# Kernel optimization log

Hardware: AMD Instinct MI355X
Metric: run time of the kernel (lower is better)

Reference implementation:

```python
import jax, jax.numpy as jnp
import numpy as np

S_LOCAL = 3
N_HEADS = 8
EPS = 1e-6


def setup_inputs() -> dict:
    key = jax.random.key(0)
    ks = jax.random.split(key, 9)
    B, D, T, H, W = 2, 512, 96, 16, 16
    std = 0.02
    return {
        "x": jax.random.normal(ks[0], (B, D, T, H, W), dtype=jnp.float32),
        "ln_gamma": jnp.ones((D,), dtype=jnp.float32),
        "ln_beta": jnp.zeros((D,), dtype=jnp.float32),
        "Wq": jax.random.normal(ks[1], (D, D), dtype=jnp.float32) * std,
        "Wk": jax.random.normal(ks[2], (D, D), dtype=jnp.float32) * std,
        "Wv": jax.random.normal(ks[3], (D, D), dtype=jnp.float32) * std,
        "Wkl": jax.random.normal(ks[4], (D, D), dtype=jnp.float32) * std,
        "Wvl": jax.random.normal(ks[5], (D, D), dtype=jnp.float32) * std,
        "Wo": jax.random.normal(ks[6], (D, D), dtype=jnp.float32) * std,
        "q_bias": jax.random.normal(ks[7], (1, N_HEADS, 1, D // N_HEADS), dtype=jnp.float32) * std,
    }


def _unfold_windows(x, s):
    # x: [..., T] -> [..., T, s] sliding windows with zero padding s//2 each side
    p = s // 2
    xp = jnp.pad(x, [(0, 0)] * (x.ndim - 1) + [(p, p)])
    T = x.shape[-1]
    idx = jnp.arange(T)[:, None] + jnp.arange(s)[None, :]  # [T, s]
    return xp[..., idx]


def reference(x, ln_gamma, ln_beta, Wq, Wk, Wv, Wkl, Wvl, Wo, q_bias):
    B, D, T, H, W = x.shape
    nh, dh, s = N_HEADS, D // N_HEADS, S_LOCAL
    factor = dh ** (-0.5)
    N = B * H * W

    # [B,D,T,H,W] -> [N, T, D]
    xt = jnp.transpose(x, (0, 3, 4, 2, 1)).reshape(N, T, D)

    # LayerNorm over D
    mu = xt.mean(-1, keepdims=True)
    var = xt.var(-1, keepdims=True)
    xn = (xt - mu) / jnp.sqrt(var + EPS) * ln_gamma + ln_beta

    # projections -> [N, nh, T, dh]
    def heads(y):
        return jnp.transpose(y.reshape(N, T, nh, dh), (0, 2, 1, 3))

    q = heads(xn @ Wq.T) + q_bias
    k = heads(xn @ Wk.T)
    v = heads(xn @ Wv.T)

    # global attention scores [N, nh, T, T]
    attn_global = jnp.einsum('bhnd,bhgd->bhng', q, k) * factor

    # local k/v: [N, T, D] -> [N, D, T] -> windows [N, D, T, s]
    kl = jnp.transpose(xn @ Wkl.T, (0, 2, 1))
    vl = jnp.transpose(xn @ Wvl.T, (0, 2, 1))
    k_w = jnp.transpose(_unfold_windows(kl, s).reshape(N, nh, dh, T, s), (0, 1, 3, 2, 4))  # [N,nh,T,dh,s]
    v_w = jnp.transpose(_unfold_windows(vl, s).reshape(N, nh, dh, T, s), (0, 1, 3, 2, 4))

    # local mask: True where window element came from zero padding -> [T, s]
    mask_local = _unfold_windows(jnp.ones((T,), dtype=jnp.float32), s) == 0

    attn_local = jnp.einsum('bhnd,bhndl->bhnl', q, k_w)
    attn_local = jnp.where(mask_local, -jnp.inf, attn_local) * factor

    # joint softmax over [T global + s local]
    attn_map = jax.nn.softmax(jnp.concatenate([attn_global, attn_local], axis=-1), axis=-1)
    ag, al = attn_map[..., :T], attn_map[..., T:]

    x_global = jnp.einsum('bhng,bhgd->bhnd', ag, v)
    x_local = jnp.einsum('bhnl,bhndl->bhnd', al, v_w)

    out = (jnp.transpose(x_global + x_local, (0, 2, 1, 3)).reshape(N, T, D)) @ Wo.T
    return jnp.transpose(out.reshape(B, H, W, T, D), (0, 4, 3, 1, 2))
```

## Files before the change

kernel.cpp:

```cpp
#include <hip/hip_runtime.h>
#include <hip/hip_fp16.h>
#include <cstdint>
#include <cstddef>

typedef _Float16 f16;
typedef _Float16 half8 __attribute__((ext_vector_type(8)));
typedef _Float16 half4v __attribute__((ext_vector_type(4)));
typedef float floatx4 __attribute__((ext_vector_type(4)));

#define MTOT 49152
#define QSCALE 0.180336880111120426f

__device__ __forceinline__ void gload_lds16(const f16* g, f16* l) {
  __builtin_amdgcn_global_load_lds((const __attribute__((address_space(1))) void*)g,
                                   (__attribute__((address_space(3))) void*)l, 16, 0, 0);
}

__device__ __forceinline__ half8 load_h8u(const f16* p) {
  half8 v;
  __builtin_memcpy(&v, p, 16);
  return v;
}

__global__ __launch_bounds__(256) void wconv_kernel(
    const float* __restrict__ Wq, const float* __restrict__ Wk,
    const float* __restrict__ Wv, const float* __restrict__ Wkl,
    const float* __restrict__ Wvl, const float* __restrict__ Wo,
    f16* __restrict__ WQKV, f16* __restrict__ WO) {
  int idx = blockIdx.x * 256 + threadIdx.x;
  if (idx < 2560 * 512) {
    int row = idx >> 9;
    int col = idx & 511;
    int seg = row >> 9;
    int r = row & 511;
    const float* src;
    switch (seg) {
      case 0: src = Wq; break;
      case 1: src = Wk; break;
      case 2: src = Wkl; break;
      case 3: src = Wvl; break;
      default: src = Wv; break;
    }
    WQKV[idx] = (f16)src[r * 512 + col];
  }
  if (idx < 512 * 512) WO[idx] = (f16)Wo[idx];
}

__global__ __launch_bounds__(256) void ln_kernel(
    const float* __restrict__ x, const float* __restrict__ gamma,
    const float* __restrict__ beta, f16* __restrict__ XN) {
  const int hwg = blockIdx.x & 3;
  const int t   = (blockIdx.x >> 2) % 96;
  const int b   = blockIdx.x / (4 * 96);
  const int lhw = threadIdx.x & 63;
  const int dg  = threadIdx.x >> 6;
  const float* xp = x + (size_t)b * 512 * 24576 + (size_t)t * 256 +
                    (hwg * 64 + lhw) + (size_t)dg * 128 * 24576;

  float v[128];
  float s = 0.f, s2 = 0.f;
#pragma unroll
  for (int j = 0; j < 128; ++j) {
    float u = xp[(size_t)j * 24576];
    v[j] = u;
    s += u;
    s2 += u * u;
  }
  __shared__ float S1[4][64], S2[4][64];
  __shared__ __align__(16) f16 XT[64][512];
  S1[dg][lhw] = s;
  S2[dg][lhw] = s2;
  __syncthreads();
  s  = S1[0][lhw] + S1[1][lhw] + S1[2][lhw] + S1[3][lhw];
  s2 = S2[0][lhw] + S2[1][lhw] + S2[2][lhw] + S2[3][lhw];
  const float mean = s * (1.f / 512.f);
  float var = s2 * (1.f / 512.f) - mean * mean;
  var = fmaxf(var, 0.f);
  const float rstd = rsqrtf(var + 1e-6f);

#pragma unroll
  for (int ic = 0; ic < 16; ++ic) {
    const int c = dg * 16 + ic;
    const int slot = c ^ (lhw & 7);
    half8 buf;
#pragma unroll
    for (int j = 0; j < 8; ++j) {
      const int d = c * 8 + j;
      buf[j] = (f16)((v[ic * 8 + j] - mean) * rstd * gamma[d] + beta[d]);
    }
    *(half8*)(&XT[lhw][slot * 8]) = buf;
  }
  __syncthreads();

  const int rr = threadIdx.x >> 2;
  const int seg = threadIdx.x & 3;
  const int n = b * 256 + hwg * 64 + rr;
  f16* outp = XN + ((size_t)n * 96 + t) * 512;
#pragma unroll
  for (int i = 0; i < 16; ++i) {
    const int c = i * 4 + seg;
    const int slot = c ^ (rr & 7);
    half8 w = *(const half8*)(&XT[rr][slot * 8]);
    *(half8*)(outp + c * 8) = w;
  }
}

__global__ __launch_bounds__(512, 2) void gemmA_kernel(
    const f16* __restrict__ A, const f16* __restrict__ B,
    f16* __restrict__ Cqkv, const float* __restrict__ qbias) {
  __shared__ f16 LA[2][256 * 64];
  __shared__ f16 LB[2][256 * 64];
  __shared__ __align__(16) f16 esc[8][16][72];

  const int lin = blockIdx.x;
  const int cpx = (int)gridDim.x >> 3;
  const int swz = (lin & 7) * cpx + (lin >> 3);
  const int o = ((gridDim.x & 7) == 0) ? swz : lin;
  const int mt = o / 10;
  const int nt = o % 10;
  const int m0 = mt * 256;
  const int n0 = nt * 256;

  const int tid = threadIdx.x;
  const int wid = tid >> 6;
  const int lane = tid & 63;
  const int wm = wid >> 2;
  const int wn = wid & 3;
  const int l15 = lane & 15, l4 = lane >> 4;

  const int srow = tid >> 3;
  const int scol = ((tid & 7) ^ (srow & 7)) * 8;
  const f16* Abase = A + (size_t)(m0 + srow) * 512 + scol;
  const f16* Bbase = B + (size_t)(n0 + srow) * 512 + scol;

  const int cks0 = ((l4) ^ (l15 & 7)) * 8;
  const int cks1 = ((4 + l4) ^ (l15 & 7)) * 8;
  const int arow = wm * 128 + l15;
  const int brow = wn * 64 + l15;

  floatx4 acc[8][4] = {};
  half8 a_f[4][2];
  half8 b_f[4][2];

  auto stageH = [&](int slot, int kt, int mat, int h) {
    const f16* g = (mat ? Bbase : Abase) + kt * 64 + (size_t)(h * 128) * 512;
    f16* l = (mat ? LB[slot] : LA[slot]) + h * 8192 + tid * 8;
    gload_lds16(g, l);
    gload_lds16(g + (size_t)64 * 512, l + 4096);
  };

  stageH(0, 0, 0, 0); stageH(0, 0, 0, 1);
  stageH(0, 0, 1, 0); stageH(0, 0, 1, 1);
  stageH(1, 1, 0, 0);
  asm volatile("s_waitcnt vmcnt(2)" ::: "memory");
  __builtin_amdgcn_s_barrier();

#pragma unroll
  for (int kt = 0; kt < 8; ++kt) {
    const f16* As = LA[kt & 1];
    const f16* Bs = LB[kt & 1];
    const int nsl = (kt + 1) & 1;

#pragma unroll
    for (int mf2 = 0; mf2 < 4; ++mf2) {
      a_f[mf2][0] = *(const half8*)(As + (arow + mf2 * 16) * 64 + cks0);
      a_f[mf2][1] = *(const half8*)(As + (arow + mf2 * 16) * 64 + cks1);
    }
#pragma unroll
    for (int nf = 0; nf < 2; ++nf) {
      b_f[nf][0] = *(const half8*)(Bs + (brow + nf * 16) * 64 + cks0);
      b_f[nf][1] = *(const half8*)(Bs + (brow + nf * 16) * 64 + cks1);
    }
    if (kt + 1 < 8) stageH(nsl, kt + 1, 0, 1);
    __builtin_amdgcn_s_barrier();
    __builtin_amdgcn_s_setprio(1);
#pragma unroll
    for (int mf2 = 0; mf2 < 4; ++mf2)
#pragma unroll
      for (int nf2 = 0; nf2 < 2; ++nf2)
#pragma unroll
        for (int ks = 0; ks < 2; ++ks)
          acc[mf2][nf2] = __builtin_amdgcn_mfma_f32_16x16x32_f16(
              a_f[mf2][ks], b_f[nf2][ks], acc[mf2][nf2], 0, 0, 0);
    __builtin_amdgcn_s_setprio(0);
    __builtin_amdgcn_s_barrier();

#pragma unroll
    for (int nf = 2; nf < 4; ++nf) {
      b_f[nf][0] = *(const half8*)(Bs + (brow + nf * 16) * 64 + cks0);
      b_f[nf][1] = *(const half8*)(Bs + (brow + nf * 16) * 64 + cks1);
    }
    if (kt + 1 < 8) stageH(nsl, kt + 1, 1, 0);
    __builtin_amdgcn_s_barrier();
    __builtin_amdgcn_s_setprio(1);
#pragma unroll
    for (int mf2 = 0; mf2 < 4; ++mf2)
#pragma unroll
      for (int nf2 = 0; nf2 < 2; ++nf2)
#pragma unroll
        for (int ks = 0; ks < 2; ++ks)
          acc[mf2][2 + nf2] = __builtin_amdgcn_mfma_f32_16x16x32_f16(
              a_f[mf2][ks], b_f[2 + nf2][ks], acc[mf2][2 + nf2], 0, 0, 0);
    __builtin_amdgcn_s_setprio(0);
    __builtin_amdgcn_s_barrier();

#pragma unroll
    for (int mf2 = 0; mf2 < 4; ++mf2) {
      a_f[mf2][0] = *(const half8*)(As + (arow + 64 + mf2 * 16) * 64 + cks0);
      a_f[mf2][1] = *(const half8*)(As + (arow + 64 + mf2 * 16) * 64 + cks1);
    }
    if (kt + 1 < 8) stageH(nsl, kt + 1, 1, 1);
    __builtin_amdgcn_s_barrier();
    __builtin_amdgcn_s_setprio(1);
#pragma unroll
    for (int mf2 = 0; mf2 < 4; ++mf2)
#pragma unroll
      for (int nf2 = 0; nf2 < 2; ++nf2)
#pragma unroll
        for (int ks = 0; ks < 2; ++ks)
          acc[4 + mf2][nf2] = __builtin_amdgcn_mfma_f32_16x16x32_f16(
              a_f[mf2][ks], b_f[nf2][ks], acc[4 + mf2][nf2], 0, 0, 0);
    __builtin_amdgcn_s_setprio(0);
    __builtin_amdgcn_s_barrier();

    if (kt + 2 < 8) stageH(kt & 1, kt + 2, 0, 0);
    __builtin_amdgcn_s_barrier();
    __builtin_amdgcn_s_setprio(1);
#pragma unroll
    for (int mf2 = 0; mf2 < 4; ++mf2)
#pragma unroll
      for (int nf2 = 0; nf2 < 2; ++nf2)
#pragma unroll
        for (int ks = 0; ks < 2; ++ks)
          acc[4 + mf2][2 + nf2] = __builtin_amdgcn_mfma_f32_16x16x32_f16(
              a_f[mf2][ks], b_f[2 + nf2][ks], acc[4 + mf2][2 + nf2], 0, 0, 0);
    __builtin_amdgcn_s_setprio(0);
    if (kt < 6) {
      asm volatile("s_waitcnt vmcnt(2)" ::: "memory");
    } else if (kt == 6) {
      asm volatile("s_waitcnt vmcnt(0)" ::: "memory");
    }
    __builtin_amdgcn_s_barrier();
  }

  float bias[4], scl[4];
#pragma unroll
  for (int nf = 0; nf < 4; ++nf) {
    const int n = n0 + wn * 64 + nf * 16 + l15;
    const bool isq = (n < 512);
    bias[nf] = isq ? qbias[n] : 0.0f;
    scl[nf]  = isq ? QSCALE : 1.0f;
  }
  const int rrow = lane >> 2;
  const int rcg  = lane & 3;
#pragma unroll
  for (int mf = 0; mf < 8; ++mf) {
#pragma unroll
    for (int nf = 0; nf < 4; ++nf)
#pragma unroll
      for (int j = 0; j < 4; ++j)
        esc[wid][l4 * 4 + j][nf * 16 + l15] = (f16)((acc[mf][nf][j] + bias[nf]) * scl[nf]);
    asm volatile("s_waitcnt lgkmcnt(0)" ::: "memory");
    half8 v0 = *(const half8*)(&esc[wid][rrow][rcg * 16]);
    half8 v1 = *(const half8*)(&esc[wid][rrow][rcg * 16 + 8]);
    asm volatile("" ::: "memory");
    f16* dst = Cqkv + (size_t)(m0 + wm * 128 + mf * 16 + rrow) * 2560 + n0 + wn * 64 + rcg * 16;
    *(half8*)dst = v0;
    *(half8*)(dst + 8) = v1;
  }
}

__global__ __launch_bounds__(256) void gemmO_kernel(
    const f16* __restrict__ A, const f16* __restrict__ B,
    float* __restrict__ Out) {
  __shared__ f16 As[2][128 * 32];
  __shared__ f16 Bs[2][128 * 32];

  const int lin = blockIdx.x;
  const int cpx = (int)gridDim.x >> 3;
  const int o = (lin & 7) * cpx + (lin >> 3);
  const int nt = o >> 2;
  const int mt = o & 3;
  const int m0 = mt * 128;
  const int n0 = nt * 128;
  const int tid = threadIdx.x;
  const int lane = tid & 63;
  const int wid = tid >> 6;
  const int wm = wid >> 1, wn = wid & 1;
  const int l15 = lane & 15, l4 = lane >> 4;

  floatx4 acc[4][4] = {};

  const int srow = tid >> 2;
  const int skp = (((tid & 3) ^ ((tid >> 3) & 3))) * 8;
  const f16* ap = A + (size_t)(m0 + srow) * 512 + skp;
  const f16* bp = B + (size_t)(n0 + srow) * 512 + skp;

  auto stage = [&](int buf, int k0) {
    f16* asl = As[buf] + tid * 8;
    f16* bsl = Bs[buf] + tid * 8;
    gload_lds16(ap + k0, asl);
    gload_lds16(ap + (size_t)64 * 512 + k0, asl + 2048);
    gload_lds16(bp + k0, bsl);
    gload_lds16(bp + (size_t)64 * 512 + k0, bsl + 2048);
  };

  const int rc = (l4 ^ ((l15 >> 1) & 3)) * 8;

  stage(0, 0);
  __syncthreads();
  int cur = 0;
  for (int k0 = 0; k0 < 512; k0 += 32) {
    if (k0 + 32 < 512) stage(cur ^ 1, k0 + 32);
    half8 af[4], bf[4];
#pragma unroll
    for (int mf = 0; mf < 4; ++mf)
      af[mf] = *(const half8*)(As[cur] + (wm * 64 + mf * 16 + l15) * 32 + rc);
#pragma unroll
    for (int nf = 0; nf < 4; ++nf)
      bf[nf] = *(const half8*)(Bs[cur] + (wn * 64 + nf * 16 + l15) * 32 + rc);
#pragma unroll
    for (int mf = 0; mf < 4; ++mf)
#pragma unroll
      for (int nf = 0; nf < 4; ++nf)
        acc[mf][nf] = __builtin_amdgcn_mfma_f32_16x16x32_f16(af[mf], bf[nf], acc[mf][nf], 0, 0, 0);
    __syncthreads();
    cur ^= 1;
  }

  const int mbase = m0 + wm * 64;
  const int nbase = n0 + wn * 64;
#pragma unroll
  for (int nf = 0; nf < 4; ++nf) {
    const int m2 = nbase + nf * 16 + l15;
    const int bb = m2 / 24576;
    const int rem = m2 - bb * 24576;
    const int t = rem >> 8;
    const int hw = rem & 255;
    float* op = Out + ((size_t)bb * 512 * 96 + t) * 256 + hw;
#pragma unroll
    for (int mf = 0; mf < 4; ++mf) {
#pragma unroll
      for (int j = 0; j < 4; ++j) {
        const int d = mbase + mf * 16 + l4 * 4 + j;
        __builtin_nontemporal_store(acc[mf][nf][j], op + (size_t)d * 24576);
      }
    }
  }
}

__global__ __launch_bounds__(192) void attn_kernel(
    const f16* __restrict__ QKV, f16* __restrict__ AO, int n0chunk) {
  const int nn = blockIdx.x >> 3;
  const int h = blockIdx.x & 7;
  const int tid = threadIdx.x;
  const int wid = tid >> 6;
  const int lane = tid & 63;
  const int l15 = lane & 15, l4 = lane >> 4;
  const int nglob = n0chunk + nn;
  const int bb = nglob >> 8, hw = nglob & 255;

  __shared__ __align__(16) f16 VTl[64][112];
  __shared__ __align__(16) f16 VLTl[64][112];
  __shared__ __align__(16) float locS[3][16][4];
  __shared__ __align__(16) f16 pS[3][16][104];
  __shared__ __align__(16) f16 pS2[3][16][40];
  __shared__ __align__(16) f16 oesc[3][16][72];

  const f16* base = QKV + (size_t)nn * 96 * 2560;

#pragma unroll
  for (int it = 0; it < 4; ++it) {
    const int r = (tid >> 3) + it * 24;
    const int c0 = (tid & 7) * 8;
    half8 v  = *(const half8*)(base + (size_t)r * 2560 + 2048 + h * 64 + c0);
    half8 vl = *(const half8*)(base + (size_t)r * 2560 + 1536 + h * 64 + c0);
#pragma unroll
    for (int j = 0; j < 8; ++j) {
      VTl[c0 + j][r]  = v[j];
      VLTl[c0 + j][r] = vl[j];
    }
  }
  if (tid < 128) {
    half8 z = {};
    *(half8*)(&VLTl[tid >> 1][96 + (tid & 1) * 8]) = z;
  }

  half8 kb[6][2];
#pragma unroll
  for (int nf = 0; nf < 6; ++nf)
#pragma unroll
    for (int kg = 0; kg < 2; ++kg)
      kb[nf][kg] = *(const half8*)(base + (size_t)(nf * 16 + l15) * 2560 + 512 + h * 64 + kg * 32 + l4 * 8);

  __syncthreads();

  for (int mb = wid * 2; mb < wid * 2 + 2; ++mb) {
    const int t0 = mb * 16;
    const int tb = (t0 >= 2) ? (t0 - 2) : 0;
    const int d0 = t0 - 1 - tb;

    half8 aq[2], kl1[2], kl2[2];
    {
      int r1 = t0 - 1 + l15; if (r1 < 0) r1 = 0;
      int r2 = t0 + 1 + l15; if (r2 > 95) r2 = 95;
#pragma unroll
      for (int kg = 0; kg < 2; ++kg) {
        aq[kg]  = *(const half8*)(base + (size_t)(t0 + l15) * 2560 + h * 64 + kg * 32 + l4 * 8);
        kl1[kg] = *(const half8*)(base + (size_t)r1 * 2560 + 1024 + h * 64 + kg * 32 + l4 * 8);
        kl2[kg] = *(const half8*)(base + (size_t)r2 * 2560 + 1024 + h * 64 + kg * 32 + l4 * 8);
      }
    }

    floatx4 s[6] = {};
    floatx4 sl1 = {}, sl2 = {};
#pragma unroll
    for (int nf = 0; nf < 6; ++nf)
#pragma unroll
      for (int kg = 0; kg < 2; ++kg)
        s[nf] = __builtin_amdgcn_mfma_f32_16x16x32_f16(aq[kg], kb[nf][kg], s[nf], 0, 0, 0);
#pragma unroll
    for (int kg = 0; kg < 2; ++kg) {
      sl1 = __builtin_amdgcn_mfma_f32_16x16x32_f16(aq[kg], kl1[kg], sl1, 0, 0, 0);
      sl2 = __builtin_amdgcn_mfma_f32_16x16x32_f16(aq[kg], kl2[kg], sl2, 0, 0, 0);
    }

    half8 vb[4][3], vlb[4];
#pragma unroll
    for (int nf = 0; nf < 4; ++nf) {
#pragma unroll
      for (int kg = 0; kg < 3; ++kg)
        vb[nf][kg] = *(const half8*)(&VTl[nf * 16 + l15][kg * 32 + l4 * 8]);
      vlb[nf] = load_h8u(&VLTl[nf * 16 + l15][tb + l4 * 8]);
    }

    {
      half8 z = {};
      f16* pz = &pS2[wid][0][0];
      *(half8*)(pz + lane * 8) = z;
      if (lane < 16) *(half8*)(pz + 512 + lane * 8) = z;
    }
#pragma unroll
    for (int j = 0; j < 4; ++j) {
      const int r = l4 * 4 + j;
      const int s1i = l15 - r;
      if (s1i >= 0 && s1i < 3) locS[wid][r][s1i] = sl1[j];
      const int s2i = l15 + 2 - r;
      if (l15 >= 14 && s2i >= 0 && s2i < 3) locS[wid][r][s2i] = sl2[j];
    }
    __syncthreads();

#pragma unroll
    for (int j = 0; j < 4; ++j) {
      const int row = l4 * 4 + j;
      float sv[6];
#pragma unroll
      for (int nf = 0; nf < 6; ++nf) sv[nf] = s[nf][j];
      float mx = sv[0];
#pragma unroll
      for (int nf = 1; nf < 6; ++nf) mx = fmaxf(mx, sv[nf]);
      for (int off = 1; off < 16; off <<= 1) mx = fmaxf(mx, __shfl_xor(mx, off, 64));
      const float l0 = (t0 + row >= 1)  ? locS[wid][row][0] : -__builtin_inff();
      const float l1 = locS[wid][row][1];
      const float l2 = (t0 + row <= 94) ? locS[wid][row][2] : -__builtin_inff();
      mx = fmaxf(mx, fmaxf(l0, fmaxf(l1, l2)));
      float e[6], sum = 0.f;
#pragma unroll
      for (int nf = 0; nf < 6; ++nf) {
        e[nf] = exp2f(sv[nf] - mx);
        sum += e[nf];
      }
      for (int off = 1; off < 16; off <<= 1) sum += __shfl_xor(sum, off, 64);
      const float e0 = exp2f(l0 - mx), e1 = exp2f(l1 - mx), e2 = exp2f(l2 - mx);
      sum += e0 + e1 + e2;
      const float rd = 1.0f / sum;
#pragma unroll
      for (int nf = 0; nf < 6; ++nf) pS[wid][row][nf * 16 + l15] = (f16)(e[nf] * rd);
      if (l15 < 3) {
        const int w = row + l15 + d0;
        const float ev = (l15 == 0) ? e0 : ((l15 == 1) ? e1 : e2);
        if (w >= 0) pS2[wid][row][w] = (f16)(ev * rd);
      }
    }
    __syncthreads();

    floatx4 o[4] = {};
    half8 pfr[3];
#pragma unroll
    for (int kg = 0; kg < 3; ++kg)
      pfr[kg] = *(const half8*)(&pS[wid][l15][kg * 32 + l4 * 8]);
    half8 pf2 = *(const half8*)(&pS2[wid][l15][l4 * 8]);
#pragma unroll
    for (int nf = 0; nf < 4; ++nf) {
#pragma unroll
      for (int kg = 0; kg < 3; ++kg)
        o[nf] = __builtin_amdgcn_mfma_f32_16x16x32_f16(pfr[kg], vb[nf][kg], o[nf], 0, 0, 0);
      o[nf] = __builtin_amdgcn_mfma_f32_16x16x32_f16(pf2, vlb[nf], o[nf], 0, 0, 0);
    }

#pragma unroll
    for (int nf = 0; nf < 4; ++nf)
#pragma unroll
      for (int j = 0; j < 4; ++j)
        oesc[wid][l4 * 4 + j][nf * 16 + l15] = (f16)o[nf][j];
    asm volatile("s_waitcnt lgkmcnt(0)" ::: "memory");
    {
      const int rrow = lane >> 2;
      const int rcg  = lane & 3;
      half8 v0 = *(const half8*)(&oesc[wid][rrow][rcg * 16]);
      half8 v1 = *(const half8*)(&oesc[wid][rrow][rcg * 16 + 8]);
      asm volatile("" ::: "memory");
      f16* dst = AO + ((size_t)(bb * 96 + t0 + rrow) * 256 + hw) * 512 + h * 64 + rcg * 16;
      *(half8*)dst = v0;
      *(half8*)(dst + 8) = v1;
    }
  }
}

extern "C" void kernel_launch(void* const* d_in, const int* in_sizes, int n_in,
                              void* d_out, int out_size, void* d_ws, size_t ws_size,
                              hipStream_t stream) {
  (void)in_sizes; (void)n_in; (void)out_size;
  const float* x     = (const float*)d_in[0];
  const float* gamma = (const float*)d_in[1];
  const float* beta  = (const float*)d_in[2];
  const float* Wq    = (const float*)d_in[3];
  const float* Wk    = (const float*)d_in[4];
  const float* Wv    = (const float*)d_in[5];
  const float* Wkl   = (const float*)d_in[6];
  const float* Wvl   = (const float*)d_in[7];
  const float* Wo    = (const float*)d_in[8];
  const float* qb    = (const float*)d_in[9];
  float* out = (float*)d_out;

  char* ws = (char*)d_ws;
  size_t off = 0;
  auto alloc = [&](size_t bytes) -> void* {
    void* p = ws + off;
    off += (bytes + 255) & ~(size_t)255;
    return p;
  };
  f16* XN   = (f16*)alloc((size_t)MTOT * 512 * 2);
  f16* AO   = (f16*)alloc((size_t)MTOT * 512 * 2);
  f16* WQKV = (f16*)alloc((size_t)2560 * 512 * 2);
  f16* WOh  = (f16*)alloc((size_t)512 * 512 * 2);
  int cn = 512;
  while (cn > 32 && off + (size_t)cn * 96 * 2560 * 2 + 256 > ws_size)
    cn >>= 1;
  f16* QKVc = (f16*)alloc((size_t)cn * 96 * 2560 * 2);

  wconv_kernel<<<5120, 256, 0, stream>>>(Wq, Wk, Wv, Wkl, Wvl, Wo, WQKV, WOh);
  ln_kernel<<<768, 256, 0, stream>>>(x, gamma, beta, XN);

  const int nch = 512 / cn;
  for (int c = 0; c < nch; ++c) {
    const int mtiles = (cn * 96) / 256;
    gemmA_kernel<<<mtiles * 10, 512, 0, stream>>>(XN + (size_t)c * cn * 96 * 512,
                                                  WQKV, QKVc, qb);
    attn_kernel<<<cn * 8, 192, 0, stream>>>(QKVc, AO, c * cn);
  }
  gemmO_kernel<<<1536, 256, 0, stream>>>(WOh, AO, out);
}
```

Baseline: 384.8 us.

## Replace output projection GEMM with 256x256-tile, 8-wave pipelined kernel

```diff
diff --git a/kernel.cpp b/kernel.cpp
--- a/kernel.cpp
+++ b/kernel.cpp
@@ -270,79 +270,155 @@
   }
 }
 
-__global__ __launch_bounds__(256) void gemmO_kernel(
+__global__ __launch_bounds__(512, 2) void gemmO256_kernel(
     const f16* __restrict__ A, const f16* __restrict__ B,
     float* __restrict__ Out) {
-  __shared__ f16 As[2][128 * 32];
-  __shared__ f16 Bs[2][128 * 32];
+  __shared__ f16 LA[2][256 * 64];
+  __shared__ f16 LB[2][256 * 64];
 
   const int lin = blockIdx.x;
   const int cpx = (int)gridDim.x >> 3;
   const int o = (lin & 7) * cpx + (lin >> 3);
-  const int nt = o >> 2;
-  const int mt = o & 3;
-  const int m0 = mt * 128;
-  const int n0 = nt * 128;
+  const int mt = o & 1;
+  const int nt = o >> 1;
+  const int m0 = mt * 256;
+  const int n0 = nt * 256;
+
   const int tid = threadIdx.x;
+  const int wid = tid >> 6;
   const int lane = tid & 63;
-  const int wid = tid >> 6;
-  const int wm = wid >> 1, wn = wid & 1;
+  const int wm = wid >> 2;
+  const int wn = wid & 3;
   const int l15 = lane & 15, l4 = lane >> 4;
 
-  floatx4 acc[4][4] = {};
-
-  const int srow = tid >> 2;
-  const int skp = (((tid & 3) ^ ((tid >> 3) & 3))) * 8;
-  const f16* ap = A + (size_t)(m0 + srow) * 512 + skp;
-  const f16* bp = B + (size_t)(n0 + srow) * 512 + skp;
-
-  auto stage = [&](int buf, int k0) {
-    f16* asl = As[buf] + tid * 8;
-    f16* bsl = Bs[buf] + tid * 8;
-    gload_lds16(ap + k0, asl);
-    gload_lds16(ap + (size_t)64 * 512 + k0, asl + 2048);
-    gload_lds16(bp + k0, bsl);
-    gload_lds16(bp + (size_t)64 * 512 + k0, bsl + 2048);
+  const int srow = tid >> 3;
+  const int scol = ((tid & 7) ^ (srow & 7)) * 8;
+  const f16* Abase = A + (size_t)(m0 + srow) * 512 + scol;
+  const f16* Bbase = B + (size_t)(n0 + srow) * 512 + scol;
+
+  const int cks0 = ((l4) ^ (l15 & 7)) * 8;
+  const int cks1 = ((4 + l4) ^ (l15 & 7)) * 8;
+  const int arow = wm * 128 + l15;
+  const int brow = wn * 64 + l15;
+
+  floatx4 acc[8][4] = {};
+  half8 a_f[4][2];
+  half8 b_f[4][2];
+
+  auto stageH = [&](int slot, int kt, int mat, int h) {
+    const f16* g = (mat ? Bbase : Abase) + kt * 64 + (size_t)(h * 128) * 512;
+    f16* l = (mat ? LB[slot] : LA[slot]) + h * 8192 + tid * 8;
+    gload_lds16(g, l);
+    gload_lds16(g + (size_t)64 * 512, l + 4096);
   };
 
-  const int rc = (l4 ^ ((l15 >> 1) & 3)) * 8;
-
-  stage(0, 0);
-  __syncthreads();
-  int cur = 0;
-  for (int k0 = 0; k0 < 512; k0 += 32) {
-    if (k0 + 32 < 512) stage(cur ^ 1, k0 + 32);
-    half8 af[4], bf[4];
-#pragma unroll
-    for (int mf = 0; mf < 4; ++mf)
-      af[mf] = *(const half8*)(As[cur] + (wm * 64 + mf * 16 + l15) * 32 + rc);
-#pragma unroll
-    for (int nf = 0; nf < 4; ++nf)
-      bf[nf] = *(const half8*)(Bs[cur] + (wn * 64 + nf * 16 + l15) * 32 + rc);
-#pragma unroll
-    for (int mf = 0; mf < 4; ++mf)
-#pragma unroll
-      for (int nf = 0; nf < 4; ++nf)
-        acc[mf][nf] = __builtin_amdgcn_mfma_f32_16x16x32_f16(af[mf], bf[nf], acc[mf][nf], 0, 0, 0);
-    __syncthreads();
-    cur ^= 1;
-  }
-
-  const int mbase = m0 + wm * 64;
-  const int nbase = n0 + wn * 64;
+  stageH(0, 0, 0, 0); stageH(0, 0, 0, 1);
+  stageH(0, 0, 1, 0); stageH(0, 0, 1, 1);
+  stageH(1, 1, 0, 0);
+  asm volatile("s_waitcnt vmcnt(2)" ::: "memory");
+  __builtin_amdgcn_s_barrier();
+
+#pragma unroll
+  for (int kt = 0; kt < 8; ++kt) {
+    const f16* As = LA[kt & 1];
+    const f16* Bs = LB[kt & 1];
+    const int nsl = (kt + 1) & 1;
+
+#pragma unroll
+    for (int mf2 = 0; mf2 < 4; ++mf2) {
+      a_f[mf2][0] = *(const half8*)(As + (arow + mf2 * 16) * 64 + cks0);
+      a_f[mf2][1] = *(const half8*)(As + (arow + mf2 * 16) * 64 + cks1);
+    }
+#pragma unroll
+    for (int nf = 0; nf < 2; ++nf) {
+      b_f[nf][0] = *(const half8*)(Bs + (brow + nf * 16) * 64 + cks0);
+      b_f[nf][1] = *(const half8*)(Bs + (brow + nf * 16) * 64 + cks1);
+    }
+    if (kt + 1 < 8) stageH(nsl, kt + 1, 0, 1);
+    __builtin_amdgcn_s_barrier();
+    __builtin_amdgcn_s_setprio(1);
+#pragma unroll
+    for (int mf2 = 0; mf2 < 4; ++mf2)
+#pragma unroll
+      for (int nf2 = 0; nf2 < 2; ++nf2)
+#pragma unroll
+        for (int ks = 0; ks < 2; ++ks)
+          acc[mf2][nf2] = __builtin_amdgcn_mfma_f32_16x16x32_f16(
+              a_f[mf2][ks], b_f[nf2][ks], acc[mf2][nf2], 0, 0, 0);
+    __builtin_amdgcn_s_setprio(0);
+    __builtin_amdgcn_s_barrier();
+
+#pragma unroll
+    for (int nf = 2; nf < 4; ++nf) {
+      b_f[nf][0] = *(const half8*)(Bs + (brow + nf * 16) * 64 + cks0);
+      b_f[nf][1] = *(const half8*)(Bs + (brow + nf * 16) * 64 + cks1);
+    }
+    if (kt + 1 < 8) stageH(nsl, kt + 1, 1, 0);
+    __builtin_amdgcn_s_barrier();
+    __builtin_amdgcn_s_setprio(1);
+#pragma unroll
+    for (int mf2 = 0; mf2 < 4; ++mf2)
+#pragma unroll
+      for (int nf2 = 0; nf2 < 2; ++nf2)
+#pragma unroll
+        for (int ks = 0; ks < 2; ++ks)
+          acc[mf2][2 + nf2] = __builtin_amdgcn_mfma_f32_16x16x32_f16(
+              a_f[mf2][ks], b_f[2 + nf2][ks], acc[mf2][2 + nf2], 0, 0, 0);
+    __builtin_amdgcn_s_setprio(0);
+    __builtin_amdgcn_s_barrier();
+
+#pragma unroll
+    for (int mf2 = 0; mf2 < 4; ++mf2) {
+      a_f[mf2][0] = *(const half8*)(As + (arow + 64 + mf2 * 16) * 64 + cks0);
+      a_f[mf2][1] = *(const half8*)(As + (arow + 64 + mf2 * 16) * 64 + cks1);
+    }
+    if (kt + 1 < 8) stageH(nsl, kt + 1, 1, 1);
+    __builtin_amdgcn_s_barrier();
+    __builtin_amdgcn_s_setprio(1);
+#pragma unroll
+    for (int mf2 = 0; mf2 < 4; ++mf2)
+#pragma unroll
+      for (int nf2 = 0; nf2 < 2; ++nf2)
+#pragma unroll
+        for (int ks = 0; ks < 2; ++ks)
+          acc[4 + mf2][nf2] = __builtin_amdgcn_mfma_f32_16x16x32_f16(
+              a_f[mf2][ks], b_f[nf2][ks], acc[4 + mf2][nf2], 0, 0, 0);
+    __builtin_amdgcn_s_setprio(0);
+    __builtin_amdgcn_s_barrier();
+
+    if (kt + 2 < 8) stageH(kt & 1, kt + 2, 0, 0);
+    __builtin_amdgcn_s_barrier();
+    __builtin_amdgcn_s_setprio(1);
+#pragma unroll
+    for (int mf2 = 0; mf2 < 4; ++mf2)
+#pragma unroll
+      for (int nf2 = 0; nf2 < 2; ++nf2)
+#pragma unroll
+        for (int ks = 0; ks < 2; ++ks)
+          acc[4 + mf2][2 + nf2] = __builtin_amdgcn_mfma_f32_16x16x32_f16(
+              a_f[mf2][ks], b_f[2 + nf2][ks], acc[4 + mf2][2 + nf2], 0, 0, 0);
+    __builtin_amdgcn_s_setprio(0);
+    if (kt < 6) {
+      asm volatile("s_waitcnt vmcnt(2)" ::: "memory");
+    } else if (kt == 6) {
+      asm volatile("s_waitcnt vmcnt(0)" ::: "memory");
+    }
+    __builtin_amdgcn_s_barrier();
+  }
+
 #pragma unroll
   for (int nf = 0; nf < 4; ++nf) {
-    const int m2 = nbase + nf * 16 + l15;
+    const int m2 = n0 + wn * 64 + nf * 16 + l15;
     const int bb = m2 / 24576;
     const int rem = m2 - bb * 24576;
     const int t = rem >> 8;
     const int hw = rem & 255;
     float* op = Out + ((size_t)bb * 512 * 96 + t) * 256 + hw;
 #pragma unroll
-    for (int mf = 0; mf < 4; ++mf) {
+    for (int mf = 0; mf < 8; ++mf) {
 #pragma unroll
       for (int j = 0; j < 4; ++j) {
-        const int d = mbase + mf * 16 + l4 * 4 + j;
+        const int d = m0 + wm * 128 + mf * 16 + l4 * 4 + j;
         __builtin_nontemporal_store(acc[mf][nf][j], op + (size_t)d * 24576);
       }
     }
@@ -559,5 +635,5 @@
                                                   WQKV, QKVc, qb);
     attn_kernel<<<cn * 8, 192, 0, stream>>>(QKVc, AO, c * cn);
   }
-  gemmO_kernel<<<1536, 256, 0, stream>>>(WOh, AO, out);
-}
+  gemmO256_kernel<<<384, 512, 0, stream>>>(WOh, AO, out);
+}
```

Measured after the change: 381.3 us. About the same (-0.9%).
